# Performance work log

Hardware: AMD Instinct MI355X
Metric: run time of the kernel (lower is better)

## Reference

```python
import jax, jax.numpy as jnp
import numpy as np

T_THRESH = 1.0  # t_thresh init arg


def _step_fn(x):
    # Heaviside forward (gradient handled separately in bwd module)
    return (x > 0).astype(x.dtype)


def setup_inputs() -> dict:
    key = jax.random.key(0)
    k1, = jax.random.split(key, 1)
    x = jax.random.normal(k1, (64, 500, 1024), dtype=jnp.float32)
    w_input = jnp.asarray(1.0, dtype=jnp.float32)
    w_leak = jnp.asarray(0.1, dtype=jnp.float32)
    return {"x": x, "w_input": w_input, "w_leak": w_leak}


def reference(x, w_input, w_leak):
    # Leaky integrate-and-fire over time axis (axis=1).
    # Vm_t = relu(w_i * x_t + (1 - w_l) * Vm_{t-1} * step(t_thresh - Vm_{t-1}))
    # spike_t = step(Vm_t - t_thresh)
    def step(Vm, xt):  # Vm, xt: [B, C]
        forget = _step_fn(T_THRESH - Vm)  # reset if Vm crossed threshold
        Vm = jax.nn.relu(w_input * xt + (1.0 - w_leak) * Vm * forget)
        spike = _step_fn(Vm - T_THRESH)
        return Vm, spike

    Vm0 = jnp.zeros_like(x[:, 0])  # [B, C]
    xt = jnp.swapaxes(x, 0, 1)  # [T, B, C]
    _, spikes = jax.lax.scan(step, Vm0, xt)
    return jnp.swapaxes(spikes, 0, 1)  # [B, T, C]
```

## Files before the change

kernel.cpp:

```cpp
#include <hip/hip_runtime.h>


#define LIF_B 64
#define LIF_T 500
#define LIF_C 1024
#define LIF_TC 25
#define LIF_NCH (LIF_T / LIF_TC)
#define LIF_BC 256

#define GLOBAL_AS(p) ((__attribute__((address_space(1))) const void*)(uintptr_t)(p))
#define LDS_AS(p)    ((__attribute__((address_space(3))) void*)(uintptr_t)(p))

__global__ __launch_bounds__(256) void lif_kernel(
    const float* __restrict__ x,
    const float* __restrict__ w_input_p,
    const float* __restrict__ w_leak_p,
    float* __restrict__ out) {

  __shared__ float lds[2][LIF_TC * LIF_BC];

  const int b     = blockIdx.x >> 2;
  const int cbase = (blockIdx.x & 3) << 8;
  const int tidx  = threadIdx.x;
  const int wave  = tidx >> 6;
  const int lane  = tidx & 63;

  const float wi = w_input_p[0];
  const float kl = __fsub_rn(1.0f, w_leak_p[0]);

  const float* xblk = x   + (size_t)b * LIF_T * LIF_C + cbase;
  float*       oblk = out + (size_t)b * LIF_T * LIF_C + cbase;

  auto stage = [&](int k, int p) {
    const float* src0 = xblk + (size_t)k * LIF_TC * LIF_C;
#pragma unroll
    for (int r0 = 0; r0 < LIF_TC; r0 += 4) {
      const int r = r0 + wave;
      if (r < LIF_TC) {
        const float* g = src0 + (size_t)r * LIF_C + lane * 4;
        float* l = &lds[p][r * LIF_BC];
        __builtin_amdgcn_global_load_lds(GLOBAL_AS(g), LDS_AS(l), 16, 0, 0);
      }
    }
  };

  stage(0, 0);

  float Vm = 0.0f;

  for (int k = 0; k < LIF_NCH; ++k) {
    const int p = k & 1;
    __syncthreads();
    if (k + 1 < LIF_NCH) stage(k + 1, p ^ 1);

    float* orow = oblk + (size_t)k * LIF_TC * LIF_C + tidx;
#pragma unroll
    for (int r = 0; r < LIF_TC; ++r) {
      const float xt  = lds[p][r * LIF_BC + tidx];
      const float acc = (Vm < 1.0f) ? __fmul_rn(kl, Vm) : 0.0f;
      const float v   = __fadd_rn(__fmul_rn(wi, xt), acc);
      Vm = fmaxf(v, 0.0f);
      orow[(size_t)r * LIF_C] = (Vm > 1.0f) ? 1.0f : 0.0f;
    }
  }
}

extern "C" void kernel_launch(void* const* d_in, const int* in_sizes, int n_in,
                              void* d_out, int out_size, void* d_ws, size_t ws_size,
                              hipStream_t stream) {
  const float* x  = (const float*)d_in[0];
  const float* wi = (const float*)d_in[1];
  const float* wl = (const float*)d_in[2];
  float* out = (float*)d_out;

  const int grid = LIF_B * (LIF_C / LIF_BC);
  lif_kernel<<<grid, 256, 0, stream>>>(x, wi, wl, out);
}
```

Baseline: 231.5 us.

## Triple-buffer per-wave LDS staging with vmcnt waits instead of block barriers

Restructures the time-chunk pipeline to three LDS buffers with a prefetch depth of two chunks, and shrinks the chunk to 20 timesteps. Each wave now loads only its own 64 channels, which lets explicit s_waitcnt vmcnt counts replace __syncthreads. Output stores become nontemporal. The waits depend on exact in-flight counts of loads and stores, so the code is fragile if the compiler reorders or merges memory operations.

```diff
diff --git a/kernel.cpp b/kernel.cpp
--- a/kernel.cpp
+++ b/kernel.cpp
@@ -4,12 +4,15 @@
 #define LIF_B 64
 #define LIF_T 500
 #define LIF_C 1024
-#define LIF_TC 25
+#define LIF_TC 20
 #define LIF_NCH (LIF_T / LIF_TC)
-#define LIF_BC 256
+#define LIF_NBUF 3
 
 #define GLOBAL_AS(p) ((__attribute__((address_space(1))) const void*)(uintptr_t)(p))
 #define LDS_AS(p)    ((__attribute__((address_space(3))) void*)(uintptr_t)(p))
+
+#define VMWAIT(n) \
+  asm volatile("s_waitcnt vmcnt(" #n ") lgkmcnt(0)" ::: "memory")
 
 __global__ __launch_bounds__(256) void lif_kernel(
     const float* __restrict__ x,
@@ -17,7 +20,7 @@
     const float* __restrict__ w_leak_p,
     float* __restrict__ out) {
 
-  __shared__ float lds[2][LIF_TC * LIF_BC];
+  __shared__ float lds[LIF_NBUF][4][LIF_TC * 64];
 
   const int b     = blockIdx.x >> 2;
   const int cbase = (blockIdx.x & 3) << 8;
@@ -27,42 +30,62 @@
 
   const float wi = w_input_p[0];
   const float kl = __fsub_rn(1.0f, w_leak_p[0]);
+  asm volatile("s_waitcnt vmcnt(0) lgkmcnt(0)" ::: "memory");
 
   const float* xblk = x   + (size_t)b * LIF_T * LIF_C + cbase;
   float*       oblk = out + (size_t)b * LIF_T * LIF_C + cbase;
 
   auto stage = [&](int k, int p) {
-    const float* src0 = xblk + (size_t)k * LIF_TC * LIF_C;
+    const float* src0 = xblk + (size_t)k * LIF_TC * LIF_C
+                      + (wave << 6) + ((lane & 15) << 2);
 #pragma unroll
     for (int r0 = 0; r0 < LIF_TC; r0 += 4) {
-      const int r = r0 + wave;
-      if (r < LIF_TC) {
-        const float* g = src0 + (size_t)r * LIF_C + lane * 4;
-        float* l = &lds[p][r * LIF_BC];
-        __builtin_amdgcn_global_load_lds(GLOBAL_AS(g), LDS_AS(l), 16, 0, 0);
-      }
+      const float* g = src0 + (size_t)(r0 + (lane >> 4)) * LIF_C;
+      float* l = &lds[p][wave][r0 * 64];
+      __builtin_amdgcn_global_load_lds(GLOBAL_AS(g), LDS_AS(l), 16, 0, 0);
     }
+    __builtin_amdgcn_sched_barrier(0);
+  };
+
+  float Vm = 0.0f;
+
+  auto compute = [&](int k, int p) {
+    float* orow = oblk + (size_t)k * LIF_TC * LIF_C + tidx;
+#pragma unroll
+    for (int r = 0; r < LIF_TC; ++r) {
+      const float xt  = lds[p][wave][r * 64 + lane];
+      const float acc = (Vm < 1.0f) ? __fmul_rn(kl, Vm) : 0.0f;
+      const float v   = __fadd_rn(__fmul_rn(wi, xt), acc);
+      Vm = fmaxf(v, 0.0f);
+      __builtin_nontemporal_store((Vm > 1.0f) ? 1.0f : 0.0f,
+                                  orow + (size_t)r * LIF_C);
+    }
+    __builtin_amdgcn_sched_barrier(0);
   };
 
   stage(0, 0);
+  stage(1, 1);
 
-  float Vm = 0.0f;
+  VMWAIT(5);
+  stage(2, 2);
+  compute(0, 0);
 
-  for (int k = 0; k < LIF_NCH; ++k) {
-    const int p = k & 1;
-    __syncthreads();
-    if (k + 1 < LIF_NCH) stage(k + 1, p ^ 1);
+  VMWAIT(25);
+  stage(3, 0);
+  compute(1, 1);
 
-    float* orow = oblk + (size_t)k * LIF_TC * LIF_C + tidx;
-#pragma unroll
-    for (int r = 0; r < LIF_TC; ++r) {
-      const float xt  = lds[p][r * LIF_BC + tidx];
-      const float acc = (Vm < 1.0f) ? __fmul_rn(kl, Vm) : 0.0f;
-      const float v   = __fadd_rn(__fmul_rn(wi, xt), acc);
-      Vm = fmaxf(v, 0.0f);
-      orow[(size_t)r * LIF_C] = (Vm > 1.0f) ? 1.0f : 0.0f;
-    }
+#pragma unroll 3
+  for (int k = 2; k <= LIF_NCH - 3; ++k) {
+    VMWAIT(45);
+    stage(k + 2, (k + 2) % LIF_NBUF);
+    compute(k, k % LIF_NBUF);
   }
+
+  VMWAIT(45);
+  compute(LIF_NCH - 2, 2);
+
+  VMWAIT(40);
+  compute(LIF_NCH - 1, 0);
 }
 
 extern "C" void kernel_launch(void* const* d_in, const int* in_sizes, int n_in,
@@ -73,6 +96,6 @@
   const float* wl = (const float*)d_in[2];
   float* out = (float*)d_out;
 
-  const int grid = LIF_B * (LIF_C / LIF_BC);
+  const int grid = LIF_B * (LIF_C / 256);
   lif_kernel<<<grid, 256, 0, stream>>>(x, wi, wl, out);
 }
```

Result: no change. 233.2 us (+0.7%).

## Warp-specialize LIF kernel with producer waves and 4-deep LDS pipeline

Applied to the files above, without the earlier changes.

Splits each 512-thread block into four producer waves that issue async global-to-LDS loads three chunks ahead and four consumer waves that run the recurrence. The buffer goes from two to four stages, synchronised with explicit vmcnt waits and raw barriers. Consumers transpose spikes through a small LDS scratch so each store is a 16-byte nontemporal write instead of a scalar store. The aim is to hide load latency behind the serial time loop and to make output stores wider. The cost is more threads per block, hand-managed waitcnt logic and an extra LDS round trip per output.

```diff
diff --git a/kernel.cpp b/kernel.cpp
--- a/kernel.cpp
+++ b/kernel.cpp
@@ -4,63 +4,91 @@
 #define LIF_B 64
 #define LIF_T 500
 #define LIF_C 1024
-#define LIF_TC 25
-#define LIF_NCH (LIF_T / LIF_TC)
-#define LIF_BC 256
+#define LIF_TC 20
+#define LIF_NCH 25
+#define LIF_NBUF 4
+
+typedef float vfloat4 __attribute__((ext_vector_type(4)));
 
 #define GLOBAL_AS(p) ((__attribute__((address_space(1))) const void*)(uintptr_t)(p))
 #define LDS_AS(p)    ((__attribute__((address_space(3))) void*)(uintptr_t)(p))
 
-__global__ __launch_bounds__(256) void lif_kernel(
+#define VMWAIT(n) asm volatile("s_waitcnt vmcnt(" #n ")" ::: "memory")
+#define LGKM0()   asm volatile("s_waitcnt lgkmcnt(0)" ::: "memory")
+#define BARRIER() do { __builtin_amdgcn_s_barrier(); asm volatile("" ::: "memory"); } while (0)
+
+__global__ __launch_bounds__(512) void lif_kernel(
     const float* __restrict__ x,
     const float* __restrict__ w_input_p,
     const float* __restrict__ w_leak_p,
     float* __restrict__ out) {
 
-  __shared__ float lds[2][LIF_TC * LIF_BC];
+  __shared__ __align__(16) float lds_x[LIF_NBUF][4][LIF_TC * 64];
+  __shared__ __align__(16) float sp[4][4 * 64];
 
   const int b     = blockIdx.x >> 2;
   const int cbase = (blockIdx.x & 3) << 8;
   const int tidx  = threadIdx.x;
   const int wave  = tidx >> 6;
   const int lane  = tidx & 63;
+  const bool producer = wave < 4;
+  const int w = wave & 3;
 
   const float wi = w_input_p[0];
   const float kl = __fsub_rn(1.0f, w_leak_p[0]);
+  asm volatile("s_waitcnt vmcnt(0) lgkmcnt(0)" ::: "memory");
 
   const float* xblk = x   + (size_t)b * LIF_T * LIF_C + cbase;
   float*       oblk = out + (size_t)b * LIF_T * LIF_C + cbase;
 
   auto stage = [&](int k, int p) {
-    const float* src0 = xblk + (size_t)k * LIF_TC * LIF_C;
+    const float* src0 = xblk + (size_t)k * LIF_TC * LIF_C
+                      + (w << 6) + ((lane & 15) << 2);
 #pragma unroll
     for (int r0 = 0; r0 < LIF_TC; r0 += 4) {
-      const int r = r0 + wave;
-      if (r < LIF_TC) {
-        const float* g = src0 + (size_t)r * LIF_C + lane * 4;
-        float* l = &lds[p][r * LIF_BC];
-        __builtin_amdgcn_global_load_lds(GLOBAL_AS(g), LDS_AS(l), 16, 0, 0);
-      }
+      const float* g = src0 + (size_t)(r0 + (lane >> 4)) * LIF_C;
+      float* l = &lds_x[p][w][r0 * 64];
+      __builtin_amdgcn_global_load_lds(GLOBAL_AS(g), LDS_AS(l), 16, 0, 0);
     }
+    __builtin_amdgcn_sched_barrier(0);
   };
-
-  stage(0, 0);
 
   float Vm = 0.0f;
 
+  if (producer) { stage(0, 0); stage(1, 1); stage(2, 2); }
+
   for (int k = 0; k < LIF_NCH; ++k) {
-    const int p = k & 1;
-    __syncthreads();
-    if (k + 1 < LIF_NCH) stage(k + 1, p ^ 1);
+    if (producer) {
+      if (k <= LIF_NCH - 3)      VMWAIT(10);
+      else if (k == LIF_NCH - 2) VMWAIT(5);
+      else                       VMWAIT(0);
+    } else {
+      LGKM0();
+    }
+    BARRIER();
 
-    float* orow = oblk + (size_t)k * LIF_TC * LIF_C + tidx;
+    if (producer) {
+      if (k + 3 < LIF_NCH) stage(k + 3, (k + 3) & 3);
+    } else {
+      const int p = k & 3;
+      float* obase = oblk + (size_t)k * LIF_TC * LIF_C + (w << 6);
 #pragma unroll
-    for (int r = 0; r < LIF_TC; ++r) {
-      const float xt  = lds[p][r * LIF_BC + tidx];
-      const float acc = (Vm < 1.0f) ? __fmul_rn(kl, Vm) : 0.0f;
-      const float v   = __fadd_rn(__fmul_rn(wi, xt), acc);
-      Vm = fmaxf(v, 0.0f);
-      orow[(size_t)r * LIF_C] = (Vm > 1.0f) ? 1.0f : 0.0f;
+      for (int r0 = 0; r0 < LIF_TC; r0 += 4) {
+#pragma unroll
+        for (int dr = 0; dr < 4; ++dr) {
+          const float xt  = lds_x[p][w][(r0 + dr) * 64 + lane];
+          const float acc = (Vm < 1.0f) ? __fmul_rn(kl, Vm) : 0.0f;
+          const float v   = __fadd_rn(__fmul_rn(wi, xt), acc);
+          Vm = fmaxf(v, 0.0f);
+          sp[w][dr * 64 + lane] = (Vm > 1.0f) ? 1.0f : 0.0f;
+        }
+        const vfloat4 v4 =
+            *reinterpret_cast<const vfloat4*>(&sp[w][lane << 2]);
+        float* gdst = obase + (size_t)(r0 + (lane >> 4)) * LIF_C
+                    + ((lane & 15) << 2);
+        __builtin_nontemporal_store(v4, reinterpret_cast<vfloat4*>(gdst));
+      }
+      __builtin_amdgcn_sched_barrier(0);
     }
   }
 }
@@ -73,6 +101,6 @@
   const float* wl = (const float*)d_in[2];
   float* out = (float*)d_out;
 
-  const int grid = LIF_B * (LIF_C / LIF_BC);
-  lif_kernel<<<grid, 256, 0, stream>>>(x, wi, wl, out);
+  const int grid = LIF_B * (LIF_C / 256);
+  lif_kernel<<<grid, 512, 0, stream>>>(x, wi, wl, out);
 }
```

New measurement: 233.7 us. No clear change (+0.9%).
